# Performance work log

Hardware: AMD Instinct MI355X
Metric: run time of the kernel (lower is better)

Reference implementation:

```python
import jax, jax.numpy as jnp
from jax import lax
import numpy as np
import math

EPS = 1e-5
NBINS = 17   # quantized color levels round(x*255/16) for x in [0,1)
K_MODE = 11

def _bn(x, g, b):
    # BatchNorm2d in training mode: batch statistics over (B,H,W)
    m = jnp.mean(x, axis=(0, 2, 3), keepdims=True)
    v = jnp.var(x, axis=(0, 2, 3), keepdims=True)
    return (x - m) * lax.rsqrt(v + EPS) * g[None, :, None, None] + b[None, :, None, None]

def _lrelu(x):
    return jnp.where(x >= 0, x, 0.01 * x)

def _shared_conv(x, w, b, stride, padding):
    # one KxK kernel shared depthwise across all channels, scalar bias
    C = x.shape[1]
    k = jnp.tile(w[None, None], (C, 1, 1, 1))  # (C,1,K,K)
    y = lax.conv_general_dilated(x, k, (stride, stride),
                                 [(padding, padding), (padding, padding)],
                                 dimension_numbers=('NCHW', 'OIHW', 'NCHW'),
                                 feature_group_count=C)
    return y + b[0]

def _avg_pool_same(x, k):
    # avg_pool2d(k, stride=1, padding=k//2, count_include_pad=True)
    p = k // 2
    s = lax.reduce_window(x, 0.0, lax.add, (1, 1, k, k), (1, 1, 1, 1),
                          [(0, 0), (0, 0), (p, p), (p, p)])
    return s / float(k * k)

def _mode_pool(xq):
    # xq values are exact multiples of 16/256 -> recover integer bin index,
    # then mode over 11x11 window = argmax of per-bin counts (histogram).
    # torch zero-padding corresponds to bin 0; argmax first-max tie-break ->
    # smallest value, matching torch.mode.
    q = jnp.clip(jnp.round(xq * (256.0 / 16.0)).astype(jnp.int32), 0, NBINS - 1)
    pad = K_MODE // 2
    qp = jnp.pad(q, ((0, 0), (0, 0), (pad, pad), (pad, pad)))
    onehot = (qp[:, :, None] == jnp.arange(NBINS, dtype=jnp.int32)[None, None, :, None, None]).astype(jnp.float32)
    counts = lax.reduce_window(onehot, 0.0, lax.add, (1, 1, 1, K_MODE, K_MODE), (1, 1, 1, 1, 1), 'VALID')
    mode_bin = jnp.argmax(counts, axis=2)  # (B,C,H,W)
    return mode_bin.astype(xq.dtype) * (16.0 / 256.0)

def _forward(x, p_w1, p_b1, p_dw1, p_db1, p_g1, p_be1,
             p_w2, p_b2, p_dw2, p_db2, p_g2, p_be2,
             d_w, d_b, ia_w, ia_b, ia_g, ia_be,
             ib_w, ib_b, ib_g, ib_be,
             f_g1, f_be1, f_g2, f_be2):
    xq = jnp.round(x * (255.0 / 16.0)) * (16.0 / 256.0)
    xm = _mode_pool(xq)
    B, C, H, W = xm.shape
    half = p_w1.shape[0]

    # prepare: 1x1 conv -> depthwise 1x1 (per-channel scale) -> BN -> LeakyReLU, twice
    h = jnp.einsum('bchw,oc->bohw', xm, p_w1) + p_b1[None, :, None, None]
    h = h * p_dw1[None, :, None, None] + p_db1[None, :, None, None]
    h = _lrelu(_bn(h, p_g1, p_be1))
    h = jnp.einsum('bchw,oc->bohw', h, p_w2) + p_b2[None, :, None, None]
    h = h * p_dw2[None, :, None, None] + p_db2[None, :, None, None]
    h = _lrelu(_bn(h, p_g2, p_be2))

    n = int(math.floor(math.log(min(H, W), 3)))
    score = jnp.zeros((B, 2 * half, H, W), x.dtype)
    d = h
    for _ in range(n):
        d = _shared_conv(d, d_w, d_b, 3, 1)  # stride-3 downgrade
        z = jax.image.resize(d, (B, half, H, W), method='bilinear')
        a = _lrelu(_bn(_shared_conv(z, ia_w, ia_b, 1, 2), ia_g, ia_be))
        bb = _lrelu(_bn(_shared_conv(z, ib_w, ib_b, 1, 2), ib_g, ib_be))
        score = score + jnp.concatenate([a, bb], axis=1)  # Splitter + Stack(1)

    def ft(s):
        s = _bn(s, f_g1, f_be1)
        s = jnp.where(s > 0.1, 0.1 + 0.7 * (s - 0.1), s)  # MaxLeakyReLU(0.7, 0.1)
        s = _bn(s, f_g2, f_be2)
        return 2.0 * s - _avg_pool_same(s, K_MODE)  # EmphaseLocal(11): x + (x - local mean)

    score = ft(ft(ft(score)))
    return score / n

def setup_inputs() -> dict:
    key = jax.random.key(0)
    ks = jax.random.split(key, 32)
    B, Cin, H, W, half = 8, 3, 384, 384, 32
    r = lambda i, shp, s=0.1: s * jax.random.normal(ks[i], shp, dtype=jnp.float32)
    g = lambda i, shp: 1.0 + 0.1 * jax.random.normal(ks[i], shp, dtype=jnp.float32)
    return dict(
        x=jax.random.uniform(ks[0], (B, Cin, H, W), dtype=jnp.float32),
        p_w1=r(1, (half, Cin), 0.3), p_b1=r(2, (half,)),
        p_dw1=g(3, (half,)), p_db1=r(4, (half,)),
        p_g1=g(5, (half,)), p_be1=r(6, (half,)),
        p_w2=r(7, (half, half), 0.2), p_b2=r(8, (half,)),
        p_dw2=g(9, (half,)), p_db2=r(10, (half,)),
        p_g2=g(11, (half,)), p_be2=r(12, (half,)),
        d_w=r(13, (3, 3), 0.2), d_b=r(14, (1,)),
        ia_w=r(15, (5, 5), 0.2), ia_b=r(16, (1,)),
        ia_g=g(17, (half,)), ia_be=r(18, (half,)),
        ib_w=r(19, (5, 5), 0.2), ib_b=r(20, (1,)),
        ib_g=g(21, (half,)), ib_be=r(22, (half,)),
        f_g1=g(23, (2 * half,)), f_be1=r(24, (2 * half,)),
        f_g2=g(25, (2 * half,)), f_be2=r(26, (2 * half,)),
    )

def reference(x, p_w1, p_b1, p_dw1, p_db1, p_g1, p_be1,
              p_w2, p_b2, p_dw2, p_db2, p_g2, p_be2,
              d_w, d_b, ia_w, ia_b, ia_g, ia_be,
              ib_w, ib_b, ib_g, ib_be,
              f_g1, f_be1, f_g2, f_be2):
    return _forward(x, p_w1, p_b1, p_dw1, p_db1, p_g1, p_be1,
                    p_w2, p_b2, p_dw2, p_db2, p_g2, p_be2,
                    d_w, d_b, ia_w, ia_b, ia_g, ia_be,
                    ib_w, ib_b, ib_g, ib_be,
                    f_g1, f_be1, f_g2, f_be2)
```

## Files before the change

### kernel.cpp

```cpp
#include <hip/hip_runtime.h>

#define HW 147456
#define WID 384
#define NB 8
#define NPC 1179648
#define HW4 36864

static __device__ __forceinline__ float lrelu01(float v) { return v >= 0.f ? v : 0.01f * v; }
static __device__ __forceinline__ float mlrelu(float v) { return v > 0.1f ? 0.1f + 0.7f * (v - 0.1f) : v; }

__global__ __launch_bounds__(256) void mode_kernel(const float* __restrict__ x,
                                                   float* __restrict__ xm) {
  __shared__ unsigned char qt[26 * 76];
  __shared__ unsigned int cc[16 * 5 * 76];
  const int plane = blockIdx.z;
  const int x0 = blockIdx.x * 64;
  const int y0 = blockIdx.y * 16;
  const float* xp = x + (size_t)plane * HW;

  for (int i = threadIdx.x; i < 26 * 76; i += 256) {
    int r = i / 76, ccol = i - r * 76;
    int gy = y0 + r - 5, gx = x0 + ccol - 5;
    unsigned char q = 0;
    if (ccol < 74 && gy >= 0 && gy < WID && gx >= 0 && gx < WID) {
      float v = xp[gy * WID + gx];
      int qi = (int)rintf(v * 15.9375f);
      qi = qi < 0 ? 0 : (qi > 16 ? 16 : qi);
      q = (unsigned char)qi;
    }
    qt[i] = q;
  }
  __syncthreads();

  for (int i = threadIdx.x; i < 16 * 74; i += 256) {
    int yy = i / 74, col = i - yy * 74;
    unsigned int w0 = 0, w1 = 0, w2 = 0, w3 = 0, w4 = 0;
#pragma unroll
    for (int dy = 0; dy < 11; ++dy) {
      int q = qt[(yy + dy) * 76 + col];
      unsigned int inc = 1u << ((q & 3) << 3);
      int wsel = q >> 2;
      w0 += (wsel == 0) ? inc : 0u;
      w1 += (wsel == 1) ? inc : 0u;
      w2 += (wsel == 2) ? inc : 0u;
      w3 += (wsel == 3) ? inc : 0u;
      w4 += (wsel == 4) ? inc : 0u;
    }
    cc[(yy * 5 + 0) * 76 + col] = w0;
    cc[(yy * 5 + 1) * 76 + col] = w1;
    cc[(yy * 5 + 2) * 76 + col] = w2;
    cc[(yy * 5 + 3) * 76 + col] = w3;
    cc[(yy * 5 + 4) * 76 + col] = w4;
  }
  __syncthreads();

  for (int i = threadIdx.x; i < 16 * 64; i += 256) {
    int yy = i / 64, xx = i - yy * 64;
    unsigned int s0 = 0, s1 = 0, s2 = 0, s3 = 0, s4 = 0;
#pragma unroll
    for (int dx = 0; dx < 11; ++dx) {
      int col = xx + dx;
      s0 += cc[(yy * 5 + 0) * 76 + col];
      s1 += cc[(yy * 5 + 1) * 76 + col];
      s2 += cc[(yy * 5 + 2) * 76 + col];
      s3 += cc[(yy * 5 + 3) * 76 + col];
      s4 += cc[(yy * 5 + 4) * 76 + col];
    }
    unsigned int words[5] = {s0, s1, s2, s3, s4};
    int best = 0;
    unsigned int bc = s0 & 0xffu;
#pragma unroll
    for (int bin = 1; bin < 17; ++bin) {
      unsigned int cnt = (words[bin >> 2] >> ((bin & 3) * 8)) & 0xffu;
      if (cnt > bc) { bc = cnt; best = bin; }
    }
    xm[(size_t)plane * HW + (size_t)(y0 + yy) * WID + (x0 + xx)] = best * 0.0625f;
  }
}

__global__ __launch_bounds__(256) void xm_mom(const float4* __restrict__ X,
                                              float* __restrict__ part9) {
  float s0 = 0, s1 = 0, s2 = 0, m00 = 0, m01 = 0, m02 = 0, m11 = 0, m12 = 0, m22 = 0;
  const int end = (blockIdx.x + 1) * 1152;
  for (int u = blockIdx.x * 1152 + threadIdx.x; u < end; u += 256) {
    int b = u / HW4, p4 = u - b * HW4;
    const float4* base = X + (size_t)b * 3 * HW4 + p4;
    float4 a = base[0], bb = base[HW4], c = base[2 * HW4];
    s0 += a.x + a.y + a.z + a.w;
    s1 += bb.x + bb.y + bb.z + bb.w;
    s2 += c.x + c.y + c.z + c.w;
    m00 += a.x * a.x + a.y * a.y + a.z * a.z + a.w * a.w;
    m01 += a.x * bb.x + a.y * bb.y + a.z * bb.z + a.w * bb.w;
    m02 += a.x * c.x + a.y * c.y + a.z * c.z + a.w * c.w;
    m11 += bb.x * bb.x + bb.y * bb.y + bb.z * bb.z + bb.w * bb.w;
    m12 += bb.x * c.x + bb.y * c.y + bb.z * c.z + bb.w * c.w;
    m22 += c.x * c.x + c.y * c.y + c.z * c.z + c.w * c.w;
  }
  float vals[9] = {s0, s1, s2, m00, m01, m02, m11, m12, m22};
  int lane = threadIdx.x & 63, wd = threadIdx.x >> 6;
  __shared__ float red[4][9];
#pragma unroll
  for (int j = 0; j < 9; ++j) {
    float v = vals[j];
    for (int off = 32; off; off >>= 1) v += __shfl_down(v, off);
    if (lane == 0) red[wd][j] = v;
  }
  __syncthreads();
  if (threadIdx.x < 9)
    part9[blockIdx.x * 9 + threadIdx.x] =
        red[0][threadIdx.x] + red[1][threadIdx.x] + red[2][threadIdx.x] + red[3][threadIdx.x];
}

__global__ __launch_bounds__(64) void prep1_affine(const float* __restrict__ part9,
                                                   const float* __restrict__ w1,
                                                   const float* __restrict__ b1,
                                                   const float* __restrict__ dw1,
                                                   const float* __restrict__ db1,
                                                   const float* __restrict__ g,
                                                   const float* __restrict__ be,
                                                   float* __restrict__ sc,
                                                   float* __restrict__ sh) {
  __shared__ double M[9];
  if (threadIdx.x < 9) {
    double s = 0.0;
    for (int i = 0; i < 256; ++i) s += (double)part9[i * 9 + threadIdx.x];
    M[threadIdx.x] = s;
  }
  __syncthreads();
  if (threadIdx.x < 32) {
    int o = threadIdx.x;
    double dw = dw1[o];
    double a0 = (double)w1[o * 3] * dw, a1 = (double)w1[o * 3 + 1] * dw,
           a2 = (double)w1[o * 3 + 2] * dw;
    double k = (double)b1[o] * dw + (double)db1[o];
    double N = (double)NPC;
    double lin = (a0 * M[0] + a1 * M[1] + a2 * M[2]) / N;
    double mean = lin + k;
    double e2 = (a0 * a0 * M[3] + a1 * a1 * M[6] + a2 * a2 * M[8] +
                 2.0 * (a0 * a1 * M[4] + a0 * a2 * M[5] + a1 * a2 * M[7])) / N +
                2.0 * k * lin + k * k;
    double var = e2 - mean * mean;
    float rstd = rsqrtf((float)var + 1e-5f);
    float scl = rstd * g[o];
    sc[o] = scl;
    sh[o] = be[o] - (float)mean * scl;
  }
}

__global__ __launch_bounds__(256) void prep_fused(const float* __restrict__ xm,
                                                  const float* __restrict__ w1,
                                                  const float* __restrict__ b1,
                                                  const float* __restrict__ dw1,
                                                  const float* __restrict__ db1,
                                                  const float* __restrict__ P1SC,
                                                  const float* __restrict__ P1SH,
                                                  const float* __restrict__ w2,
                                                  const float* __restrict__ b2,
                                                  const float* __restrict__ dw2,
                                                  const float* __restrict__ db2,
                                                  float* __restrict__ t2,
                                                  float* __restrict__ part) {
  __shared__ float wl[1024];
  __shared__ float c1[32][4];
  __shared__ float bias2[32];
  __shared__ float wred[8][32];
  for (int i = threadIdx.x; i < 1024; i += 256) wl[i] = w2[i] * dw2[i >> 5];
  if (threadIdx.x < 32) {
    int o = threadIdx.x;
    float dw = dw1[o], s1 = P1SC[o];
    c1[o][0] = w1[o * 3] * dw * s1;
    c1[o][1] = w1[o * 3 + 1] * dw * s1;
    c1[o][2] = w1[o * 3 + 2] * dw * s1;
    c1[o][3] = (b1[o] * dw + db1[o]) * s1 + P1SH[o];
    bias2[o] = b2[o] * dw2[o] + db2[o];
  }
  __syncthreads();
  const int p0 = blockIdx.x * 512 + threadIdx.x;
  const int b = p0 / HW, pp = p0 - b * HW;
  const float* xb = xm + (size_t)b * 3 * HW + pp;
  float h[2][32];
#pragma unroll
  for (int q = 0; q < 2; ++q) {
    float x0 = xb[q * 256], x1 = xb[HW + q * 256], x2 = xb[2 * HW + q * 256];
#pragma unroll
    for (int o = 0; o < 32; ++o) {
      float u = fmaf(x0, c1[o][0], fmaf(x1, c1[o][1], fmaf(x2, c1[o][2], c1[o][3])));
      h[q][o] = lrelu01(u);
    }
  }
  float sv[32], sq[32];
  float* ob = t2 + (size_t)b * 32 * HW + pp;
  const float4* wl4 = reinterpret_cast<const float4*>(wl);
  for (int o = 0; o < 32; ++o) {
    float acc0 = bias2[o], acc1 = bias2[o];
#pragma unroll
    for (int c4 = 0; c4 < 8; ++c4) {
      float4 w4 = wl4[o * 8 + c4];
      int c = c4 * 4;
      acc0 = fmaf(h[0][c], w4.x, acc0);     acc1 = fmaf(h[1][c], w4.x, acc1);
      acc0 = fmaf(h[0][c + 1], w4.y, acc0); acc1 = fmaf(h[1][c + 1], w4.y, acc1);
      acc0 = fmaf(h[0][c + 2], w4.z, acc0); acc1 = fmaf(h[1][c + 2], w4.z, acc1);
      acc0 = fmaf(h[0][c + 3], w4.w, acc0); acc1 = fmaf(h[1][c + 3], w4.w, acc1);
    }
    ob[(size_t)o * HW] = acc0;
    ob[(size_t)o * HW + 256] = acc1;
    sv[o] = acc0 + acc1;
    sq[o] = acc0 * acc0 + acc1 * acc1;
  }
  int lane = threadIdx.x & 63, wd = threadIdx.x >> 6;
#pragma unroll
  for (int o = 0; o < 32; ++o) {
    float a = sv[o], q = sq[o];
    for (int off = 32; off; off >>= 1) {
      a += __shfl_down(a, off);
      q += __shfl_down(q, off);
    }
    if (lane == 0) { wred[wd][o] = a; wred[wd + 4][o] = q; }
  }
  __syncthreads();
  if (threadIdx.x < 32) {
    int o = threadIdx.x;
    part[((size_t)o * 2304 + blockIdx.x) * 2] = wred[0][o] + wred[1][o] + wred[2][o] + wred[3][o];
    part[((size_t)o * 2304 + blockIdx.x) * 2 + 1] = wred[4][o] + wred[5][o] + wred[6][o] + wred[7][o];
  }
}

__global__ __launch_bounds__(64) void stats_combine(const float* __restrict__ part, int nsplit,
                                                    const float* __restrict__ g,
                                                    const float* __restrict__ be,
                                                    float* __restrict__ sc,
                                                    float* __restrict__ sh) {
  const int c = blockIdx.x;
  double s = 0.0, q = 0.0;
  for (int i = threadIdx.x; i < nsplit; i += 64) {
    s += part[((size_t)c * nsplit + i) * 2];
    q += part[((size_t)c * nsplit + i) * 2 + 1];
  }
  for (int off = 32; off; off >>= 1) {
    s += __shfl_down(s, off);
    q += __shfl_down(q, off);
  }
  if (threadIdx.x == 0) {
    double mean = s / (double)NPC;
    double var = q / (double)NPC - mean * mean;
    float rstd = rsqrtf((float)var + 1e-5f);
    float scl = rstd * g[c];
    sc[c] = scl;
    sh[c] = be[c] - (float)mean * scl;
  }
}

template <bool AFF>
__global__ __launch_bounds__(256) void dconv(const float* __restrict__ in,
                                             const float* __restrict__ sc,
                                             const float* __restrict__ sh,
                                             const float* __restrict__ w9,
                                             const float* __restrict__ db,
                                             int Sin, int Sout,
                                             float* __restrict__ out, int total) {
  int idx = blockIdx.x * 256 + threadIdx.x;
  if (idx >= total) return;
  int xx = idx % Sout;
  int t = idx / Sout;
  int yy = t % Sout;
  int pc = t / Sout;
  int c = pc & 31;
  const float* ip = in + (size_t)pc * Sin * Sin;
  float a = AFF ? sc[c] : 1.f;
  float h = AFF ? sh[c] : 0.f;
  float acc = 0.f;
#pragma unroll
  for (int ky = 0; ky < 3; ++ky) {
    int iy = 3 * yy - 1 + ky;
    if (iy < 0 || iy >= Sin) continue;
#pragma unroll
    for (int kx = 0; kx < 3; ++kx) {
      int ix = 3 * xx - 1 + kx;
      if (ix < 0 || ix >= Sin) continue;
      float v = ip[(size_t)iy * Sin + ix];
      if (AFF) { v = v * a + h; v = lrelu01(v); }
      acc = fmaf(v, w9[ky * 3 + kx], acc);
    }
  }
  out[idx] = acc + db[0];
}

__device__ __forceinline__ void stage_geo2(int Sin, float scale, int tx, int ty,
                                           int* gx0, int* gx1, float* gfx, float* gxv,
                                           int* gy0, int* gy1, float* gfy, float* gyv) {
  if (threadIdx.x < 72) {
    int t = threadIdx.x >= 36 ? threadIdx.x - 36 : threadIdx.x;
    bool isY = threadIdx.x >= 36;
    int gp = (isY ? ty : tx) + t - 2;
    float valid = (gp >= 0 && gp < WID) ? 1.f : 0.f;
    int gpc = gp < 0 ? 0 : (gp >= WID ? WID - 1 : gp);
    float s = (gpc + 0.5f) * scale - 0.5f;
    float f0 = floorf(s);
    float fr = s - f0;
    int ii = (int)f0;
    int i1 = ii + 1 < Sin - 1 ? ii + 1 : Sin - 1;
    int i0 = ii > 0 ? ii : 0;
    if (isY) { gy0[t] = i0; gy1[t] = i1; gfy[t] = fr; gyv[t] = valid; }
    else     { gx0[t] = i0; gx1[t] = i1; gfx[t] = fr; gxv[t] = valid; }
  }
}

__device__ __forceinline__ void stage_sep(float* zt, float* dH, const float* dp, int Sin,
                                          const int* gx0, const int* gx1,
                                          const float* gfx, const float* gxv,
                                          const int* gy0, const int* gy1,
                                          const float* gfy, const float* gyv,
                                          int rowlo, int nrows) {
  for (int i = threadIdx.x; i < nrows * 36; i += 256) {
    int r = i / 36, zx = i - r * 36;
    const float* drow = dp + (size_t)(rowlo + r) * Sin;
    float v0 = drow[gx0[zx]], v1 = drow[gx1[zx]];
    dH[r * 40 + zx] = (v0 + gfx[zx] * (v1 - v0)) * gxv[zx];
  }
  __syncthreads();
  for (int i = threadIdx.x; i < 36 * 9; i += 256) {
    int zy = i / 9, k = i - zy * 9;
    int r0 = gy0[zy] - rowlo, r1 = gy1[zy] - rowlo;
    float fy = gfy[zy], vv = gyv[zy];
    float4 a = *reinterpret_cast<const float4*>(&dH[r0 * 40 + k * 4]);
    float4 b = *reinterpret_cast<const float4*>(&dH[r1 * 40 + k * 4]);
    float4 o;
    o.x = (a.x + fy * (b.x - a.x)) * vv;
    o.y = (a.y + fy * (b.y - a.y)) * vv;
    o.z = (a.z + fy * (b.z - a.z)) * vv;
    o.w = (a.w + fy * (b.w - a.w)) * vv;
    *reinterpret_cast<float4*>(&zt[zy * 40 + k * 4]) = o;
  }
}

__device__ __forceinline__ void conv_ab(const float* zt, int row, int g,
                                        const float* wa, const float* wb,
                                        float ba0, float bb0, float* A, float* Bv) {
  float aa0 = ba0, aa1 = ba0, aa2 = ba0, aa3 = ba0;
  float eb0 = bb0, eb1 = bb0, eb2 = bb0, eb3 = bb0;
#pragma unroll
  for (int dy = 0; dy < 5; ++dy) {
    const float* zr = &zt[(row + dy) * 40 + g * 4];
    float4 zlo = *reinterpret_cast<const float4*>(zr);
    float4 zhi = *reinterpret_cast<const float4*>(zr + 4);
    float z[8] = {zlo.x, zlo.y, zlo.z, zlo.w, zhi.x, zhi.y, zhi.z, zhi.w};
#pragma unroll
    for (int dx = 0; dx < 5; ++dx) {
      float wva = wa[dy * 5 + dx], wvb = wb[dy * 5 + dx];
      aa0 = fmaf(z[dx], wva, aa0);
      aa1 = fmaf(z[dx + 1], wva, aa1);
      aa2 = fmaf(z[dx + 2], wva, aa2);
      aa3 = fmaf(z[dx + 3], wva, aa3);
      eb0 = fmaf(z[dx], wvb, eb0);
      eb1 = fmaf(z[dx + 1], wvb, eb1);
      eb2 = fmaf(z[dx + 2], wvb, eb2);
      eb3 = fmaf(z[dx + 3], wvb, eb3);
    }
  }
  A[0] = aa0; A[1] = aa1; A[2] = aa2; A[3] = aa3;
  Bv[0] = eb0; Bv[1] = eb1; Bv[2] = eb2; Bv[3] = eb3;
}

__global__ __launch_bounds__(256) void upstats_all(const float* __restrict__ d1,
                                                   const float* __restrict__ d2,
                                                   const float* __restrict__ d3,
                                                   const float* __restrict__ d4,
                                                   const float* __restrict__ d5,
                                                   const float* __restrict__ wA5,
                                                   const float* __restrict__ wB5,
                                                   const float* __restrict__ bA,
                                                   const float* __restrict__ bB,
                                                   float* __restrict__ partA,
                                                   float* __restrict__ partB) {
  __shared__ __align__(16) float zt[36 * 40];
  __shared__ __align__(16) float dH[16 * 40];
  __shared__ int gx0[36], gx1[36], gy0[36], gy1[36];
  __shared__ float gfx[36], gfy[36], gxv[36], gyv[36];
  __shared__ float red[16];
  const int lvl = blockIdx.z;
  const float* dsel = lvl == 0 ? d1 : lvl == 1 ? d2 : lvl == 2 ? d3 : lvl == 3 ? d4 : d5;
  const int Sin = lvl == 0 ? 128 : lvl == 1 ? 43 : lvl == 2 ? 15 : lvl == 3 ? 5 : 2;
  const float scale = (float)Sin / 384.f;
  const int plane = blockIdx.y, tile = blockIdx.x;
  const int tx = (tile % 12) * 32, ty = (tile / 12) * 32;
  const float* dp = dsel + (size_t)plane * Sin * Sin;

  stage_geo2(Sin, scale, tx, ty, gx0, gx1, gfx, gxv, gy0, gy1, gfy, gyv);
  float wa[25], wb[25];
#pragma unroll
  for (int k = 0; k < 25; ++k) { wa[k] = wA5[k]; wb[k] = wB5[k]; }
  float ba0 = bA[0], bb0 = bB[0];
  __syncthreads();
  const int rowlo = gy0[0], nrows = gy1[35] - rowlo + 1;
  stage_sep(zt, dH, dp, Sin, gx0, gx1, gfx, gxv, gy0, gy1, gfy, gyv, rowlo, nrows);
  __syncthreads();

  float A[4], Bv[4];
  conv_ab(zt, threadIdx.x >> 3, threadIdx.x & 7, wa, wb, ba0, bb0, A, Bv);
  float sa = A[0] + A[1] + A[2] + A[3];
  float qa = A[0] * A[0] + A[1] * A[1] + A[2] * A[2] + A[3] * A[3];
  float sb = Bv[0] + Bv[1] + Bv[2] + Bv[3];
  float qb = Bv[0] * Bv[0] + Bv[1] * Bv[1] + Bv[2] * Bv[2] + Bv[3] * Bv[3];
  int lane = threadIdx.x & 63, wd = threadIdx.x >> 6;
  for (int off = 32; off; off >>= 1) {
    sa += __shfl_down(sa, off); qa += __shfl_down(qa, off);
    sb += __shfl_down(sb, off); qb += __shfl_down(qb, off);
  }
  if (lane == 0) {
    red[wd * 4] = sa; red[wd * 4 + 1] = qa;
    red[wd * 4 + 2] = sb; red[wd * 4 + 3] = qb;
  }
  __syncthreads();
  if (threadIdx.x == 0) {
    int b = plane >> 5, c = plane & 31;
    size_t pi = (size_t)lvl * 73728 + ((size_t)c * 1152 + (size_t)b * 144 + tile) * 2;
    partA[pi] = red[0] + red[4] + red[8] + red[12];
    partA[pi + 1] = red[1] + red[5] + red[9] + red[13];
    partB[pi] = red[2] + red[6] + red[10] + red[14];
    partB[pi + 1] = red[3] + red[7] + red[11] + red[15];
  }
}

__global__ __launch_bounds__(64) void combine_lvls(const float* __restrict__ partA,
                                                   const float* __restrict__ partB,
                                                   const float* __restrict__ ia_g,
                                                   const float* __restrict__ ia_be,
                                                   const float* __restrict__ ib_g,
                                                   const float* __restrict__ ib_be,
                                                   float* __restrict__ aff) {
  const int c = blockIdx.x, lvl = blockIdx.y, z = blockIdx.z;
  const float* part = (z ? partB : partA) + (size_t)lvl * 73728;
  const float* g = z ? ib_g : ia_g;
  const float* be = z ? ib_be : ia_be;
  double s = 0.0, q = 0.0;
  for (int i = threadIdx.x; i < 1152; i += 64) {
    s += part[((size_t)c * 1152 + i) * 2];
    q += part[((size_t)c * 1152 + i) * 2 + 1];
  }
  for (int off = 32; off; off >>= 1) {
    s += __shfl_down(s, off);
    q += __shfl_down(q, off);
  }
  if (threadIdx.x == 0) {
    double mean = s / (double)NPC;
    double var = q / (double)NPC - mean * mean;
    float rstd = rsqrtf((float)var + 1e-5f);
    float scl = rstd * g[c];
    aff[((z * 5 + lvl) * 2 + 0) * 32 + c] = scl;
    aff[((z * 5 + lvl) * 2 + 1) * 32 + c] = be[c] - (float)mean * scl;
  }
}

__global__ __launch_bounds__(256) void apply_all(const float* __restrict__ d1,
                                                 const float* __restrict__ d2,
                                                 const float* __restrict__ d3,
                                                 const float* __restrict__ d4,
                                                 const float* __restrict__ d5,
                                                 const float* __restrict__ wA5,
                                                 const float* __restrict__ wB5,
                                                 const float* __restrict__ bA,
                                                 const float* __restrict__ bB,
                                                 const float* __restrict__ aff,
                                                 float* __restrict__ outp,
                                                 float* __restrict__ partF) {
  __shared__ __align__(16) float zt[36 * 40];
  __shared__ __align__(16) float dH[16 * 40];
  __shared__ int gx0[36], gx1[36], gy0[36], gy1[36];
  __shared__ float gfx[36], gfy[36], gxv[36], gyv[36];
  __shared__ float red[16];
  const int plane = blockIdx.y, tile = blockIdx.x;
  const int tx = (tile % 12) * 32, ty = (tile / 12) * 32;
  const int b = plane >> 5, c = plane & 31;
  float wa[25], wb[25];
#pragma unroll
  for (int k = 0; k < 25; ++k) { wa[k] = wA5[k]; wb[k] = wB5[k]; }
  const float ba0 = bA[0], bb0 = bB[0];
  const int row = threadIdx.x >> 3, g = threadIdx.x & 7;

  float acA[4] = {0.f, 0.f, 0.f, 0.f}, acB[4] = {0.f, 0.f, 0.f, 0.f};
  for (int lvl = 0; lvl < 5; ++lvl) {
    const float* dsel = lvl == 0 ? d1 : lvl == 1 ? d2 : lvl == 2 ? d3 : lvl == 3 ? d4 : d5;
    const int Sin = lvl == 0 ? 128 : lvl == 1 ? 43 : lvl == 2 ? 15 : lvl == 3 ? 5 : 2;
    const float scale = (float)Sin / 384.f;
    const float* dp = dsel + (size_t)plane * Sin * Sin;
    __syncthreads();
    stage_geo2(Sin, scale, tx, ty, gx0, gx1, gfx, gxv, gy0, gy1, gfy, gyv);
    __syncthreads();
    const int rowlo = gy0[0], nrows = gy1[35] - rowlo + 1;
    stage_sep(zt, dH, dp, Sin, gx0, gx1, gfx, gxv, gy0, gy1, gfy, gyv, rowlo, nrows);
    __syncthreads();
    float A[4], Bv[4];
    conv_ab(zt, row, g, wa, wb, ba0, bb0, A, Bv);
    float as = aff[(lvl * 2 + 0) * 32 + c], ah = aff[(lvl * 2 + 1) * 32 + c];
    float bs = aff[((5 + lvl) * 2 + 0) * 32 + c], bh = aff[((5 + lvl) * 2 + 1) * 32 + c];
#pragma unroll
    for (int j = 0; j < 4; ++j) {
      acA[j] += lrelu01(fmaf(A[j], as, ah));
      acB[j] += lrelu01(fmaf(Bv[j], bs, bh));
    }
  }
  float4 xa = {acA[0], acA[1], acA[2], acA[3]};
  float4 xb = {acB[0], acB[1], acB[2], acB[3]};
  size_t po = (size_t)(b * 64 + c) * HW + (size_t)(ty + row) * WID + tx + g * 4;
  *reinterpret_cast<float4*>(outp + po) = xa;
  *reinterpret_cast<float4*>(outp + po + (size_t)32 * HW) = xb;

  float sa = xa.x + xa.y + xa.z + xa.w;
  float qa = xa.x * xa.x + xa.y * xa.y + xa.z * xa.z + xa.w * xa.w;
  float sb = xb.x + xb.y + xb.z + xb.w;
  float qb = xb.x * xb.x + xb.y * xb.y + xb.z * xb.z + xb.w * xb.w;
  int lane = threadIdx.x & 63, wd = threadIdx.x >> 6;
  for (int off = 32; off; off >>= 1) {
    sa += __shfl_down(sa, off); qa += __shfl_down(qa, off);
    sb += __shfl_down(sb, off); qb += __shfl_down(qb, off);
  }
  if (lane == 0) {
    red[wd * 4] = sa; red[wd * 4 + 1] = qa;
    red[wd * 4 + 2] = sb; red[wd * 4 + 3] = qb;
  }
  __syncthreads();
  if (threadIdx.x == 0) {
    size_t piA = ((size_t)c * 1152 + (size_t)b * 144 + tile) * 2;
    size_t piB = ((size_t)(c + 32) * 1152 + (size_t)b * 144 + tile) * 2;
    partF[piA] = red[0] + red[4] + red[8] + red[12];
    partF[piA + 1] = red[1] + red[5] + red[9] + red[13];
    partF[piB] = red[2] + red[6] + red[10] + red[14];
    partF[piB + 1] = red[3] + red[7] + red[11] + red[15];
  }
}

__global__ __launch_bounds__(256) void stats_mlrelu(const float4* __restrict__ X,
                                                    const float* __restrict__ sc1,
                                                    const float* __restrict__ sh1,
                                                    float* __restrict__ part) {
  int c = blockIdx.x >> 6, s = blockIdx.x & 63;
  float a1 = sc1[c], b1 = sh1[c];
  float sum = 0.f, sq = 0.f;
  int fi = s * 4608 + threadIdx.x;
#pragma unroll 2
  for (int it = 0; it < 18; ++it, fi += 256) {
    int b = fi / HW4, p4 = fi - b * HW4;
    float4 v = X[(size_t)(b * 64 + c) * HW4 + p4];
    float u;
    u = mlrelu(fmaf(v.x, a1, b1)); sum += u; sq += u * u;
    u = mlrelu(fmaf(v.y, a1, b1)); sum += u; sq += u * u;
    u = mlrelu(fmaf(v.z, a1, b1)); sum += u; sq += u * u;
    u = mlrelu(fmaf(v.w, a1, b1)); sum += u; sq += u * u;
  }
  int lane = threadIdx.x & 63, wd = threadIdx.x >> 6;
  for (int off = 32; off; off >>= 1) {
    sum += __shfl_down(sum, off);
    sq += __shfl_down(sq, off);
  }
  __shared__ float red[8];
  if (lane == 0) { red[wd * 2] = sum; red[wd * 2 + 1] = sq; }
  __syncthreads();
  if (threadIdx.x == 0) {
    part[((size_t)c * 64 + s) * 2] = red[0] + red[2] + red[4] + red[6];
    part[((size_t)c * 64 + s) * 2 + 1] = red[1] + red[3] + red[5] + red[7];
  }
}

__global__ __launch_bounds__(256) void ft_fused(const float* __restrict__ src,
                                                const float* __restrict__ F1SC,
                                                const float* __restrict__ F1SH,
                                                const float* __restrict__ F2SC,
                                                const float* __restrict__ F2SH,
                                                float* __restrict__ dst, float fscale,
                                                float* __restrict__ part) {
  __shared__ float sl[74 * 81];
  __shared__ __align__(16) float Hl[74 * 64];
  __shared__ float red[8];
  const int tile = blockIdx.x;
  const int plane = blockIdx.y;
  const int b = plane >> 6, c = plane & 63;
  const int tx = (tile % 6) * 64, ty = (tile / 6) * 64;
  const float a1 = F1SC[c], b1 = F1SH[c], a2 = F2SC[c], b2 = F2SH[c];
  const float* sp = src + (size_t)plane * HW;

  for (int i = threadIdx.x; i < 74 * 20; i += 256) {
    int r = i / 20, k = i - r * 20;
    int gy = ty + r - 5, gx = tx + k * 4 - 8;
    float4 sv = {0.f, 0.f, 0.f, 0.f};
    if (gy >= 0 && gy < WID && gx >= 0 && gx < WID) {
      float4 v = *reinterpret_cast<const float4*>(sp + (size_t)gy * WID + gx);
      sv.x = fmaf(mlrelu(fmaf(v.x, a1, b1)), a2, b2);
      sv.y = fmaf(mlrelu(fmaf(v.y, a1, b1)), a2, b2);
      sv.z = fmaf(mlrelu(fmaf(v.z, a1, b1)), a2, b2);
      sv.w = fmaf(mlrelu(fmaf(v.w, a1, b1)), a2, b2);
    }
    int base = r * 81 + k * 4;
    sl[base] = sv.x; sl[base + 1] = sv.y; sl[base + 2] = sv.z; sl[base + 3] = sv.w;
  }
  __syncthreads();

  for (int i = threadIdx.x; i < 74 * 16; i += 256) {
    int r = i >> 4, g = i & 15;
    const float* s0 = &sl[r * 81 + g * 4 + 3];
    float v[14];
#pragma unroll
    for (int j = 0; j < 14; ++j) v[j] = s0[j];
    float h0 = v[0] + v[1] + v[2] + v[3] + v[4] + v[5] + v[6] + v[7] + v[8] + v[9] + v[10];
    float h1 = h0 - v[0] + v[11];
    float h2 = h1 - v[1] + v[12];
    float h3 = h2 - v[2] + v[13];
    float4 hh = {h0, h1, h2, h3};
    *reinterpret_cast<float4*>(&Hl[r * 64 + g * 4]) = hh;
  }
  __syncthreads();

  const int g = threadIdx.x & 15, ly = threadIdx.x >> 4;
  const int y0 = ly * 4;
  const float4* H4 = reinterpret_cast<const float4*>(Hl);
  float4 acc = H4[y0 * 16 + g];
#pragma unroll
  for (int dy = 1; dy < 11; ++dy) {
    float4 t = H4[(y0 + dy) * 16 + g];
    acc.x += t.x; acc.y += t.y; acc.z += t.z; acc.w += t.w;
  }
  float sum = 0.f, sq = 0.f;
  float* dpo = dst + (size_t)plane * HW;
#pragma unroll
  for (int ry = 0; ry < 4; ++ry) {
    int y = y0 + ry;
    if (ry) {
      float4 ta = H4[(y + 10) * 16 + g];
      float4 tb = H4[(y - 1) * 16 + g];
      acc.x += ta.x - tb.x; acc.y += ta.y - tb.y;
      acc.z += ta.z - tb.z; acc.w += ta.w - tb.w;
    }
    const float* cp = &sl[(y + 5) * 81 + g * 4 + 8];
    float4 o;
    o.x = (2.f * cp[0] - acc.x * (1.f / 121.f)) * fscale;
    o.y = (2.f * cp[1] - acc.y * (1.f / 121.f)) * fscale;
    o.z = (2.f * cp[2] - acc.z * (1.f / 121.f)) * fscale;
    o.w = (2.f * cp[3] - acc.w * (1.f / 121.f)) * fscale;
    *reinterpret_cast<float4*>(dpo + (size_t)(ty + y) * WID + tx + g * 4) = o;
    sum += o.x + o.y + o.z + o.w;
    sq += o.x * o.x + o.y * o.y + o.z * o.z + o.w * o.w;
  }
  if (part) {
    int lane = threadIdx.x & 63, wd = threadIdx.x >> 6;
    for (int off = 32; off; off >>= 1) {
      sum += __shfl_down(sum, off);
      sq += __shfl_down(sq, off);
    }
    if (lane == 0) { red[wd * 2] = sum; red[wd * 2 + 1] = sq; }
    __syncthreads();
    if (threadIdx.x == 0) {
      size_t pi = ((size_t)c * 288 + (size_t)b * 36 + tile) * 2;
      part[pi] = red[0] + red[2] + red[4] + red[6];
      part[pi + 1] = red[1] + red[3] + red[5] + red[7];
    }
  }
}

extern "C" void kernel_launch(void* const* d_in, const int* in_sizes, int n_in,
                              void* d_out, int out_size, void* d_ws, size_t ws_size,
                              hipStream_t stream) {
  const float* x     = (const float*)d_in[0];
  const float* p_w1  = (const float*)d_in[1];
  const float* p_b1  = (const float*)d_in[2];
  const float* p_dw1 = (const float*)d_in[3];
  const float* p_db1 = (const float*)d_in[4];
  const float* p_g1  = (const float*)d_in[5];
  const float* p_be1 = (const float*)d_in[6];
  const float* p_w2  = (const float*)d_in[7];
  const float* p_b2  = (const float*)d_in[8];
  const float* p_dw2 = (const float*)d_in[9];
  const float* p_db2 = (const float*)d_in[10];
  const float* p_g2  = (const float*)d_in[11];
  const float* p_be2 = (const float*)d_in[12];
  const float* d_w   = (const float*)d_in[13];
  const float* d_b   = (const float*)d_in[14];
  const float* ia_w  = (const float*)d_in[15];
  const float* ia_b  = (const float*)d_in[16];
  const float* ia_g  = (const float*)d_in[17];
  const float* ia_be = (const float*)d_in[18];
  const float* ib_w  = (const float*)d_in[19];
  const float* ib_b  = (const float*)d_in[20];
  const float* ib_g  = (const float*)d_in[21];
  const float* ib_be = (const float*)d_in[22];
  const float* f_g1  = (const float*)d_in[23];
  const float* f_be1 = (const float*)d_in[24];
  const float* f_g2  = (const float*)d_in[25];
  const float* f_be2 = (const float*)d_in[26];
  float* out = (float*)d_out;
  float* ws = (float*)d_ws;

  const size_t SLOT = 37748736ull;
  float* B0 = ws;
  float* B1 = ws + 2 * SLOT;
  float* t2 = B0;
  float* partA = B0 + SLOT;
  float* partB = partA + 368640;
  float* partP = partB + 368640;
  float* part9 = partP + 147456;
  float* aff   = part9 + 2304;
  float* xm  = B1;
  float* dd1 = xm + 3538944;
  float* dd2 = dd1 + 4194304;
  float* dd3 = dd2 + 473344;
  float* dd4 = dd3 + 57600;
  float* dd5 = dd4 + 6400;
  float* partF = ws + 4 * SLOT;
  float* partS = partF + 147456;
  float* st    = partS + 8192;

  float* P1SC = st,       *P1SH = st + 32;
  float* P2SC = st + 64,  *P2SH = st + 96;
  float* F1SC = st + 128, *F1SH = st + 192;
  float* F2SC = st + 256, *F2SH = st + 320;

  mode_kernel<<<dim3(6, 24, 24), 256, 0, stream>>>(x, xm);
  xm_mom<<<256, 256, 0, stream>>>((const float4*)xm, part9);
  prep1_affine<<<1, 64, 0, stream>>>(part9, p_w1, p_b1, p_dw1, p_db1, p_g1, p_be1, P1SC, P1SH);
  prep_fused<<<2304, 256, 0, stream>>>(xm, p_w1, p_b1, p_dw1, p_db1, P1SC, P1SH,
                                       p_w2, p_b2, p_dw2, p_db2, t2, partP);
  stats_combine<<<32, 64, 0, stream>>>(partP, 2304, p_g2, p_be2, P2SC, P2SH);

  dconv<true><<<16384, 256, 0, stream>>>(t2, P2SC, P2SH, d_w, d_b, 384, 128, dd1,
                                         8 * 32 * 128 * 128);
  dconv<false><<<(8 * 32 * 43 * 43 + 255) / 256, 256, 0, stream>>>(
      dd1, nullptr, nullptr, d_w, d_b, 128, 43, dd2, 8 * 32 * 43 * 43);
  dconv<false><<<(8 * 32 * 15 * 15 + 255) / 256, 256, 0, stream>>>(
      dd2, nullptr, nullptr, d_w, d_b, 43, 15, dd3, 8 * 32 * 15 * 15);
  dconv<false><<<(8 * 32 * 5 * 5 + 255) / 256, 256, 0, stream>>>(
      dd3, nullptr, nullptr, d_w, d_b, 15, 5, dd4, 8 * 32 * 5 * 5);
  dconv<false><<<(8 * 32 * 2 * 2 + 255) / 256, 256, 0, stream>>>(
      dd4, nullptr, nullptr, d_w, d_b, 5, 2, dd5, 8 * 32 * 2 * 2);

  upstats_all<<<dim3(144, 256, 5), 256, 0, stream>>>(dd1, dd2, dd3, dd4, dd5,
                                                     ia_w, ib_w, ia_b, ib_b, partA, partB);
  combine_lvls<<<dim3(32, 5, 2), 64, 0, stream>>>(partA, partB, ia_g, ia_be, ib_g, ib_be, aff);
  apply_all<<<dim3(144, 256), 256, 0, stream>>>(dd1, dd2, dd3, dd4, dd5,
                                                ia_w, ib_w, ia_b, ib_b, aff, out, partF);

  const float* cur = out;
  float* dsts[3] = {B0, B1, out};
  for (int k = 0; k < 3; ++k) {
    stats_combine<<<64, 64, 0, stream>>>(partF, (k == 0) ? 1152 : 288, f_g1, f_be1, F1SC, F1SH);
    stats_mlrelu<<<64 * 64, 256, 0, stream>>>((const float4*)cur, F1SC, F1SH, partS);
    stats_combine<<<64, 64, 0, stream>>>(partS, 64, f_g2, f_be2, F2SC, F2SH);
    ft_fused<<<dim3(36, 512), 256, 0, stream>>>(cur, F1SC, F1SH, F2SC, F2SH, dsts[k],
                                                (k == 2) ? 0.2f : 1.0f,
                                                (k < 2) ? partF : nullptr);
    cur = dsts[k];
  }
}
```

Before: 2.131 ms.

## Merge pyramid stats and apply into one double-buffered, software-pipelined templated kernel

```diff
diff --git a/kernel.cpp b/kernel.cpp
--- a/kernel.cpp
+++ b/kernel.cpp
@@ -285,139 +285,234 @@
   out[idx] = acc + db[0];
 }
 
-__device__ __forceinline__ void stage_geo2(int Sin, float scale, int tx, int ty,
-                                           int* gx0, int* gx1, float* gfx, float* gxv,
-                                           int* gy0, int* gy1, float* gfy, float* gyv) {
-  if (threadIdx.x < 72) {
-    int t = threadIdx.x >= 36 ? threadIdx.x - 36 : threadIdx.x;
-    bool isY = threadIdx.x >= 36;
-    int gp = (isY ? ty : tx) + t - 2;
-    float valid = (gp >= 0 && gp < WID) ? 1.f : 0.f;
-    int gpc = gp < 0 ? 0 : (gp >= WID ? WID - 1 : gp);
-    float s = (gpc + 0.5f) * scale - 0.5f;
-    float f0 = floorf(s);
-    float fr = s - f0;
-    int ii = (int)f0;
-    int i1 = ii + 1 < Sin - 1 ? ii + 1 : Sin - 1;
-    int i0 = ii > 0 ? ii : 0;
-    if (isY) { gy0[t] = i0; gy1[t] = i1; gfy[t] = fr; gyv[t] = valid; }
-    else     { gx0[t] = i0; gx1[t] = i1; gfx[t] = fr; gxv[t] = valid; }
-  }
-}
-
-__device__ __forceinline__ void stage_sep(float* zt, float* dH, const float* dp, int Sin,
-                                          const int* gx0, const int* gx1,
-                                          const float* gfx, const float* gxv,
-                                          const int* gy0, const int* gy1,
-                                          const float* gfy, const float* gyv,
-                                          int rowlo, int nrows) {
-  for (int i = threadIdx.x; i < nrows * 36; i += 256) {
-    int r = i / 36, zx = i - r * 36;
-    const float* drow = dp + (size_t)(rowlo + r) * Sin;
-    float v0 = drow[gx0[zx]], v1 = drow[gx1[zx]];
-    dH[r * 40 + zx] = (v0 + gfx[zx] * (v1 - v0)) * gxv[zx];
-  }
-  __syncthreads();
-  for (int i = threadIdx.x; i < 36 * 9; i += 256) {
-    int zy = i / 9, k = i - zy * 9;
-    int r0 = gy0[zy] - rowlo, r1 = gy1[zy] - rowlo;
-    float fy = gfy[zy], vv = gyv[zy];
-    float4 a = *reinterpret_cast<const float4*>(&dH[r0 * 40 + k * 4]);
-    float4 b = *reinterpret_cast<const float4*>(&dH[r1 * 40 + k * 4]);
-    float4 o;
-    o.x = (a.x + fy * (b.x - a.x)) * vv;
-    o.y = (a.y + fy * (b.y - a.y)) * vv;
-    o.z = (a.z + fy * (b.z - a.z)) * vv;
-    o.w = (a.w + fy * (b.w - a.w)) * vv;
-    *reinterpret_cast<float4*>(&zt[zy * 40 + k * 4]) = o;
-  }
-}
-
-__device__ __forceinline__ void conv_ab(const float* zt, int row, int g,
-                                        const float* wa, const float* wb,
-                                        float ba0, float bb0, float* A, float* Bv) {
-  float aa0 = ba0, aa1 = ba0, aa2 = ba0, aa3 = ba0;
-  float eb0 = bb0, eb1 = bb0, eb2 = bb0, eb3 = bb0;
-#pragma unroll
-  for (int dy = 0; dy < 5; ++dy) {
-    const float* zr = &zt[(row + dy) * 40 + g * 4];
-    float4 zlo = *reinterpret_cast<const float4*>(zr);
-    float4 zhi = *reinterpret_cast<const float4*>(zr + 4);
-    float z[8] = {zlo.x, zlo.y, zlo.z, zlo.w, zhi.x, zhi.y, zhi.z, zhi.w};
-#pragma unroll
-    for (int dx = 0; dx < 5; ++dx) {
-      float wva = wa[dy * 5 + dx], wvb = wb[dy * 5 + dx];
-      aa0 = fmaf(z[dx], wva, aa0);
-      aa1 = fmaf(z[dx + 1], wva, aa1);
-      aa2 = fmaf(z[dx + 2], wva, aa2);
-      aa3 = fmaf(z[dx + 3], wva, aa3);
-      eb0 = fmaf(z[dx], wvb, eb0);
-      eb1 = fmaf(z[dx + 1], wvb, eb1);
-      eb2 = fmaf(z[dx + 2], wvb, eb2);
-      eb3 = fmaf(z[dx + 3], wvb, eb3);
-    }
-  }
-  A[0] = aa0; A[1] = aa1; A[2] = aa2; A[3] = aa3;
-  Bv[0] = eb0; Bv[1] = eb1; Bv[2] = eb2; Bv[3] = eb3;
-}
-
-__global__ __launch_bounds__(256) void upstats_all(const float* __restrict__ d1,
-                                                   const float* __restrict__ d2,
-                                                   const float* __restrict__ d3,
-                                                   const float* __restrict__ d4,
-                                                   const float* __restrict__ d5,
-                                                   const float* __restrict__ wA5,
-                                                   const float* __restrict__ wB5,
-                                                   const float* __restrict__ bA,
-                                                   const float* __restrict__ bB,
-                                                   float* __restrict__ partA,
-                                                   float* __restrict__ partB) {
-  __shared__ __align__(16) float zt[36 * 40];
-  __shared__ __align__(16) float dH[16 * 40];
-  __shared__ int gx0[36], gx1[36], gy0[36], gy1[36];
-  __shared__ float gfx[36], gfy[36], gxv[36], gyv[36];
-  __shared__ float red[16];
-  const int lvl = blockIdx.z;
-  const float* dsel = lvl == 0 ? d1 : lvl == 1 ? d2 : lvl == 2 ? d3 : lvl == 3 ? d4 : d5;
-  const int Sin = lvl == 0 ? 128 : lvl == 1 ? 43 : lvl == 2 ? 15 : lvl == 3 ? 5 : 2;
-  const float scale = (float)Sin / 384.f;
+static __device__ __forceinline__ int sin_of(int l) {
+  return l == 0 ? 128 : l == 1 ? 43 : l == 2 ? 15 : l == 3 ? 5 : 2;
+}
+
+template <bool APPLY>
+__global__ __launch_bounds__(256) void pyramid_k(
+    const float* __restrict__ d1, const float* __restrict__ d2,
+    const float* __restrict__ d3, const float* __restrict__ d4,
+    const float* __restrict__ d5,
+    const float* __restrict__ wA5, const float* __restrict__ wB5,
+    const float* __restrict__ bA, const float* __restrict__ bB,
+    const float* __restrict__ aff, float* __restrict__ outp,
+    float* __restrict__ partA, float* __restrict__ partB,
+    float* __restrict__ partF) {
+  __shared__ __align__(16) float zt[2][36 * 40];
+  __shared__ __align__(16) float dH[2][16 * 40];
+  __shared__ int gx0[2][36], gx1[2][36], gy0[2][36], gy1[2][36];
+  __shared__ float gfx[2][36], gfy[2][36], gxv[2][36], gyv[2][36];
+  __shared__ float red[80];
+  __shared__ int rowloS[2];
+
   const int plane = blockIdx.y, tile = blockIdx.x;
   const int tx = (tile % 12) * 32, ty = (tile / 12) * 32;
-  const float* dp = dsel + (size_t)plane * Sin * Sin;
-
-  stage_geo2(Sin, scale, tx, ty, gx0, gx1, gfx, gxv, gy0, gy1, gfy, gyv);
+  const int b = plane >> 5, c = plane & 31;
   float wa[25], wb[25];
 #pragma unroll
   for (int k = 0; k < 25; ++k) { wa[k] = wA5[k]; wb[k] = wB5[k]; }
-  float ba0 = bA[0], bb0 = bB[0];
-  __syncthreads();
-  const int rowlo = gy0[0], nrows = gy1[35] - rowlo + 1;
-  stage_sep(zt, dH, dp, Sin, gx0, gx1, gfx, gxv, gy0, gy1, gfy, gyv, rowlo, nrows);
-  __syncthreads();
-
-  float A[4], Bv[4];
-  conv_ab(zt, threadIdx.x >> 3, threadIdx.x & 7, wa, wb, ba0, bb0, A, Bv);
-  float sa = A[0] + A[1] + A[2] + A[3];
-  float qa = A[0] * A[0] + A[1] * A[1] + A[2] * A[2] + A[3] * A[3];
-  float sb = Bv[0] + Bv[1] + Bv[2] + Bv[3];
-  float qb = Bv[0] * Bv[0] + Bv[1] * Bv[1] + Bv[2] * Bv[2] + Bv[3] * Bv[3];
-  int lane = threadIdx.x & 63, wd = threadIdx.x >> 6;
-  for (int off = 32; off; off >>= 1) {
-    sa += __shfl_down(sa, off); qa += __shfl_down(qa, off);
-    sb += __shfl_down(sb, off); qb += __shfl_down(qb, off);
-  }
-  if (lane == 0) {
-    red[wd * 4] = sa; red[wd * 4 + 1] = qa;
-    red[wd * 4 + 2] = sb; red[wd * 4 + 3] = qb;
-  }
-  __syncthreads();
-  if (threadIdx.x == 0) {
-    int b = plane >> 5, c = plane & 31;
-    size_t pi = (size_t)lvl * 73728 + ((size_t)c * 1152 + (size_t)b * 144 + tile) * 2;
-    partA[pi] = red[0] + red[4] + red[8] + red[12];
-    partA[pi + 1] = red[1] + red[5] + red[9] + red[13];
-    partB[pi] = red[2] + red[6] + red[10] + red[14];
-    partB[pi + 1] = red[3] + red[7] + red[11] + red[15];
+  const float ba0 = bA[0], bb0 = bB[0];
+  const int row = threadIdx.x >> 3, g = threadIdx.x & 7;
+  const int lane = threadIdx.x & 63, wd = threadIdx.x >> 6;
+
+  float v0a, v1a, fxa, xva, v0b, v1b, fxb, xvb;
+  int offA, offB;
+  bool okA = false, okB = false;
+
+  auto plane_ptr = [&](int l) -> const float* {
+    const float* base = l == 0 ? d1 : l == 1 ? d2 : l == 2 ? d3 : l == 3 ? d4 : d5;
+    int Sin = sin_of(l);
+    return base + (size_t)plane * (Sin * Sin);
+  };
+
+  auto GEO = [&](int l, int s) {
+    int Sin = sin_of(l);
+    float scale = (float)Sin / 384.f;
+    if (threadIdx.x < 72) {
+      int t = threadIdx.x >= 36 ? threadIdx.x - 36 : threadIdx.x;
+      bool isY = threadIdx.x >= 36;
+      int gp = (isY ? ty : tx) + t - 2;
+      float valid = (gp >= 0 && gp < WID) ? 1.f : 0.f;
+      int gpc = gp < 0 ? 0 : (gp >= WID ? WID - 1 : gp);
+      float sp = (gpc + 0.5f) * scale - 0.5f;
+      float f0 = floorf(sp);
+      float fr = sp - f0;
+      int ii = (int)f0;
+      int i1 = ii + 1 < Sin - 1 ? ii + 1 : Sin - 1;
+      int i0 = ii > 0 ? ii : 0;
+      if (isY) {
+        gy0[s][t] = i0; gy1[s][t] = i1; gfy[s][t] = fr; gyv[s][t] = valid;
+        if (t == 0) rowloS[s] = i0;
+      } else {
+        gx0[s][t] = i0; gx1[s][t] = i1; gfx[s][t] = fr; gxv[s][t] = valid;
+      }
+    }
+  };
+
+  auto XISSUE = [&](int l, int s) {
+    int Sin = sin_of(l);
+    const float* dpl = plane_ptr(l);
+    int rl = rowloS[s];
+    int cnt = (gy1[s][35] - rl + 1) * 36;
+    int i = threadIdx.x;
+    okA = i < cnt;
+    if (okA) {
+      int r = i / 36, zx = i - r * 36;
+      const float* drow = dpl + (size_t)(rl + r) * Sin;
+      v0a = drow[gx0[s][zx]];
+      v1a = drow[gx1[s][zx]];
+      fxa = gfx[s][zx]; xva = gxv[s][zx];
+      offA = r * 40 + zx;
+    }
+    i += 256;
+    okB = i < cnt;
+    if (okB) {
+      int r = i / 36, zx = i - r * 36;
+      const float* drow = dpl + (size_t)(rl + r) * Sin;
+      v0b = drow[gx0[s][zx]];
+      v1b = drow[gx1[s][zx]];
+      fxb = gfx[s][zx]; xvb = gxv[s][zx];
+      offB = r * 40 + zx;
+    }
+  };
+
+  auto DHWRITE = [&](int s) {
+    if (okA) dH[s][offA] = (v0a + fxa * (v1a - v0a)) * xva;
+    if (okB) dH[s][offB] = (v0b + fxb * (v1b - v0b)) * xvb;
+  };
+
+  auto YINTERP = [&](int s) {
+    int rl = rowloS[s];
+    for (int i = threadIdx.x; i < 324; i += 256) {
+      int zy = i / 9, k = i - zy * 9;
+      int r0 = gy0[s][zy] - rl, r1 = gy1[s][zy] - rl;
+      float fy = gfy[s][zy], vv = gyv[s][zy];
+      float4 a4 = *reinterpret_cast<const float4*>(&dH[s][r0 * 40 + k * 4]);
+      float4 b4 = *reinterpret_cast<const float4*>(&dH[s][r1 * 40 + k * 4]);
+      float4 o;
+      o.x = (a4.x + fy * (b4.x - a4.x)) * vv;
+      o.y = (a4.y + fy * (b4.y - a4.y)) * vv;
+      o.z = (a4.z + fy * (b4.z - a4.z)) * vv;
+      o.w = (a4.w + fy * (b4.w - a4.w)) * vv;
+      *reinterpret_cast<float4*>(&zt[s][zy * 40 + k * 4]) = o;
+    }
+  };
+
+  GEO(0, 0);
+  __syncthreads();
+  XISSUE(0, 0);
+  DHWRITE(0);
+  GEO(1, 1);
+  __syncthreads();
+  YINTERP(0);
+  __syncthreads();
+
+  float acA[4] = {0.f, 0.f, 0.f, 0.f}, acB[4] = {0.f, 0.f, 0.f, 0.f};
+
+  for (int l = 0; l < 5; ++l) {
+    const int s = l & 1;
+    if (l < 4) XISSUE(l + 1, s ^ 1);
+
+    float A0 = ba0, A1 = ba0, A2 = ba0, A3 = ba0;
+    float B0 = bb0, B1 = bb0, B2 = bb0, B3 = bb0;
+#pragma unroll
+    for (int dy = 0; dy < 5; ++dy) {
+      const float* zr = &zt[s][(row + dy) * 40 + g * 4];
+      float4 zlo = *reinterpret_cast<const float4*>(zr);
+      float4 zhi = *reinterpret_cast<const float4*>(zr + 4);
+      float z[8] = {zlo.x, zlo.y, zlo.z, zlo.w, zhi.x, zhi.y, zhi.z, zhi.w};
+#pragma unroll
+      for (int dx = 0; dx < 5; ++dx) {
+        float wva = wa[dy * 5 + dx], wvb = wb[dy * 5 + dx];
+        A0 = fmaf(z[dx], wva, A0);
+        A1 = fmaf(z[dx + 1], wva, A1);
+        A2 = fmaf(z[dx + 2], wva, A2);
+        A3 = fmaf(z[dx + 3], wva, A3);
+        B0 = fmaf(z[dx], wvb, B0);
+        B1 = fmaf(z[dx + 1], wvb, B1);
+        B2 = fmaf(z[dx + 2], wvb, B2);
+        B3 = fmaf(z[dx + 3], wvb, B3);
+      }
+    }
+
+    if (APPLY) {
+      float as = aff[(l * 2 + 0) * 32 + c], ah = aff[(l * 2 + 1) * 32 + c];
+      float bs = aff[((5 + l) * 2 + 0) * 32 + c], bh = aff[((5 + l) * 2 + 1) * 32 + c];
+      acA[0] += lrelu01(fmaf(A0, as, ah));
+      acA[1] += lrelu01(fmaf(A1, as, ah));
+      acA[2] += lrelu01(fmaf(A2, as, ah));
+      acA[3] += lrelu01(fmaf(A3, as, ah));
+      acB[0] += lrelu01(fmaf(B0, bs, bh));
+      acB[1] += lrelu01(fmaf(B1, bs, bh));
+      acB[2] += lrelu01(fmaf(B2, bs, bh));
+      acB[3] += lrelu01(fmaf(B3, bs, bh));
+    } else {
+      float sa = A0 + A1 + A2 + A3;
+      float qa = A0 * A0 + A1 * A1 + A2 * A2 + A3 * A3;
+      float sb = B0 + B1 + B2 + B3;
+      float qb = B0 * B0 + B1 * B1 + B2 * B2 + B3 * B3;
+      for (int off = 32; off; off >>= 1) {
+        sa += __shfl_down(sa, off); qa += __shfl_down(qa, off);
+        sb += __shfl_down(sb, off); qb += __shfl_down(qb, off);
+      }
+      if (lane == 0) {
+        red[l * 16 + wd * 4 + 0] = sa;
+        red[l * 16 + wd * 4 + 1] = qa;
+        red[l * 16 + wd * 4 + 2] = sb;
+        red[l * 16 + wd * 4 + 3] = qb;
+      }
+    }
+
+    if (l < 4) DHWRITE(s ^ 1);
+    if (l < 3) GEO(l + 2, s);
+    if (l < 4) {
+      __syncthreads();
+      YINTERP(s ^ 1);
+      __syncthreads();
+    }
+  }
+
+  if (APPLY) {
+    float4 xa = {acA[0], acA[1], acA[2], acA[3]};
+    float4 xb = {acB[0], acB[1], acB[2], acB[3]};
+    size_t po = (size_t)(b * 64 + c) * HW + (size_t)(ty + row) * WID + tx + g * 4;
+    *reinterpret_cast<float4*>(outp + po) = xa;
+    *reinterpret_cast<float4*>(outp + po + (size_t)32 * HW) = xb;
+    float sa = xa.x + xa.y + xa.z + xa.w;
+    float qa = xa.x * xa.x + xa.y * xa.y + xa.z * xa.z + xa.w * xa.w;
+    float sb = xb.x + xb.y + xb.z + xb.w;
+    float qb = xb.x * xb.x + xb.y * xb.y + xb.z * xb.z + xb.w * xb.w;
+    for (int off = 32; off; off >>= 1) {
+      sa += __shfl_down(sa, off); qa += __shfl_down(qa, off);
+      sb += __shfl_down(sb, off); qb += __shfl_down(qb, off);
+    }
+    if (lane == 0) {
+      red[wd * 4 + 0] = sa; red[wd * 4 + 1] = qa;
+      red[wd * 4 + 2] = sb; red[wd * 4 + 3] = qb;
+    }
+    __syncthreads();
+    if (threadIdx.x == 0) {
+      size_t piA = ((size_t)c * 1152 + (size_t)b * 144 + tile) * 2;
+      size_t piB = ((size_t)(c + 32) * 1152 + (size_t)b * 144 + tile) * 2;
+      partF[piA] = red[0] + red[4] + red[8] + red[12];
+      partF[piA + 1] = red[1] + red[5] + red[9] + red[13];
+      partF[piB] = red[2] + red[6] + red[10] + red[14];
+      partF[piB + 1] = red[3] + red[7] + red[11] + red[15];
+    }
+  } else {
+    __syncthreads();
+    if (threadIdx.x < 5) {
+      int l = threadIdx.x;
+      const float* rl_ = &red[l * 16];
+      float SA = rl_[0] + rl_[4] + rl_[8] + rl_[12];
+      float QA = rl_[1] + rl_[5] + rl_[9] + rl_[13];
+      float SB = rl_[2] + rl_[6] + rl_[10] + rl_[14];
+      float QB = rl_[3] + rl_[7] + rl_[11] + rl_[15];
+      size_t pi = (size_t)l * 73728 + ((size_t)c * 1152 + (size_t)b * 144 + tile) * 2;
+      partA[pi] = SA; partA[pi + 1] = QA;
+      partB[pi] = SB; partB[pi + 1] = QB;
+    }
   }
 }
 
@@ -451,84 +546,6 @@
   }
 }
 
-__global__ __launch_bounds__(256) void apply_all(const float* __restrict__ d1,
-                                                 const float* __restrict__ d2,
-                                                 const float* __restrict__ d3,
-                                                 const float* __restrict__ d4,
-                                                 const float* __restrict__ d5,
-                                                 const float* __restrict__ wA5,
-                                                 const float* __restrict__ wB5,
-                                                 const float* __restrict__ bA,
-                                                 const float* __restrict__ bB,
-                                                 const float* __restrict__ aff,
-                                                 float* __restrict__ outp,
-                                                 float* __restrict__ partF) {
-  __shared__ __align__(16) float zt[36 * 40];
-  __shared__ __align__(16) float dH[16 * 40];
-  __shared__ int gx0[36], gx1[36], gy0[36], gy1[36];
-  __shared__ float gfx[36], gfy[36], gxv[36], gyv[36];
-  __shared__ float red[16];
-  const int plane = blockIdx.y, tile = blockIdx.x;
-  const int tx = (tile % 12) * 32, ty = (tile / 12) * 32;
-  const int b = plane >> 5, c = plane & 31;
-  float wa[25], wb[25];
-#pragma unroll
-  for (int k = 0; k < 25; ++k) { wa[k] = wA5[k]; wb[k] = wB5[k]; }
-  const float ba0 = bA[0], bb0 = bB[0];
-  const int row = threadIdx.x >> 3, g = threadIdx.x & 7;
-
-  float acA[4] = {0.f, 0.f, 0.f, 0.f}, acB[4] = {0.f, 0.f, 0.f, 0.f};
-  for (int lvl = 0; lvl < 5; ++lvl) {
-    const float* dsel = lvl == 0 ? d1 : lvl == 1 ? d2 : lvl == 2 ? d3 : lvl == 3 ? d4 : d5;
-    const int Sin = lvl == 0 ? 128 : lvl == 1 ? 43 : lvl == 2 ? 15 : lvl == 3 ? 5 : 2;
-    const float scale = (float)Sin / 384.f;
-    const float* dp = dsel + (size_t)plane * Sin * Sin;
-    __syncthreads();
-    stage_geo2(Sin, scale, tx, ty, gx0, gx1, gfx, gxv, gy0, gy1, gfy, gyv);
-    __syncthreads();
-    const int rowlo = gy0[0], nrows = gy1[35] - rowlo + 1;
-    stage_sep(zt, dH, dp, Sin, gx0, gx1, gfx, gxv, gy0, gy1, gfy, gyv, rowlo, nrows);
-    __syncthreads();
-    float A[4], Bv[4];
-    conv_ab(zt, row, g, wa, wb, ba0, bb0, A, Bv);
-    float as = aff[(lvl * 2 + 0) * 32 + c], ah = aff[(lvl * 2 + 1) * 32 + c];
-    float bs = aff[((5 + lvl) * 2 + 0) * 32 + c], bh = aff[((5 + lvl) * 2 + 1) * 32 + c];
-#pragma unroll
-    for (int j = 0; j < 4; ++j) {
-      acA[j] += lrelu01(fmaf(A[j], as, ah));
-      acB[j] += lrelu01(fmaf(Bv[j], bs, bh));
-    }
-  }
-  float4 xa = {acA[0], acA[1], acA[2], acA[3]};
-  float4 xb = {acB[0], acB[1], acB[2], acB[3]};
-  size_t po = (size_t)(b * 64 + c) * HW + (size_t)(ty + row) * WID + tx + g * 4;
-  *reinterpret_cast<float4*>(outp + po) = xa;
-  *reinterpret_cast<float4*>(outp + po + (size_t)32 * HW) = xb;
-
-  float sa = xa.x + xa.y + xa.z + xa.w;
-  float qa = xa.x * xa.x + xa.y * xa.y + xa.z * xa.z + xa.w * xa.w;
-  float sb = xb.x + xb.y + xb.z + xb.w;
-  float qb = xb.x * xb.x + xb.y * xb.y + xb.z * xb.z + xb.w * xb.w;
-  int lane = threadIdx.x & 63, wd = threadIdx.x >> 6;
-  for (int off = 32; off; off >>= 1) {
-    sa += __shfl_down(sa, off); qa += __shfl_down(qa, off);
-    sb += __shfl_down(sb, off); qb += __shfl_down(qb, off);
-  }
-  if (lane == 0) {
-    red[wd * 4] = sa; red[wd * 4 + 1] = qa;
-    red[wd * 4 + 2] = sb; red[wd * 4 + 3] = qb;
-  }
-  __syncthreads();
-  if (threadIdx.x == 0) {
-    size_t piA = ((size_t)c * 1152 + (size_t)b * 144 + tile) * 2;
-    size_t piB = ((size_t)(c + 32) * 1152 + (size_t)b * 144 + tile) * 2;
-    partF[piA] = red[0] + red[4] + red[8] + red[12];
-    partF[piA + 1] = red[1] + red[5] + red[9] + red[13];
-    partF[piB] = red[2] + red[6] + red[10] + red[14];
-    partF[piB + 1] = red[3] + red[7] + red[11] + red[15];
-  }
-}
-
 __global__ __launch_bounds__(256) void stats_mlrelu(const float4* __restrict__ X,
                                                     const float* __restrict__ sc1,
                                                     const float* __restrict__ sh1,
@@ -536,11 +553,11 @@
   int c = blockIdx.x >> 6, s = blockIdx.x & 63;
   float a1 = sc1[c], b1 = sh1[c];
   float sum = 0.f, sq = 0.f;
-  int fi = s * 4608 + threadIdx.x;
-#pragma unroll 2
-  for (int it = 0; it < 18; ++it, fi += 256) {
-    int b = fi / HW4, p4 = fi - b * HW4;
-    float4 v = X[(size_t)(b * 64 + c) * HW4 + p4];
+  int b = s >> 3;
+  const float4* Xp = X + (size_t)(b * 64 + c) * HW4 + (s & 7) * 4608 + threadIdx.x;
+#pragma unroll 6
+  for (int it = 0; it < 18; ++it) {
+    float4 v = Xp[it * 256];
     float u;
     u = mlrelu(fmaf(v.x, a1, b1)); sum += u; sq += u * u;
     u = mlrelu(fmaf(v.y, a1, b1)); sum += u; sq += u * u;
@@ -730,11 +747,13 @@
   dconv<false><<<(8 * 32 * 2 * 2 + 255) / 256, 256, 0, stream>>>(
       dd4, nullptr, nullptr, d_w, d_b, 5, 2, dd5, 8 * 32 * 2 * 2);
 
-  upstats_all<<<dim3(144, 256, 5), 256, 0, stream>>>(dd1, dd2, dd3, dd4, dd5,
-                                                     ia_w, ib_w, ia_b, ib_b, partA, partB);
+  pyramid_k<false><<<dim3(144, 256), 256, 0, stream>>>(
+      dd1, dd2, dd3, dd4, dd5, ia_w, ib_w, ia_b, ib_b,
+      nullptr, nullptr, partA, partB, nullptr);
   combine_lvls<<<dim3(32, 5, 2), 64, 0, stream>>>(partA, partB, ia_g, ia_be, ib_g, ib_be, aff);
-  apply_all<<<dim3(144, 256), 256, 0, stream>>>(dd1, dd2, dd3, dd4, dd5,
-                                                ia_w, ib_w, ia_b, ib_b, aff, out, partF);
+  pyramid_k<true><<<dim3(144, 256), 256, 0, stream>>>(
+      dd1, dd2, dd3, dd4, dd5, ia_w, ib_w, ia_b, ib_b,
+      aff, out, nullptr, nullptr, partF);
 
   const float* cur = out;
   float* dsts[3] = {B0, B1, out};
```

Result: slower. 2.416 ms (+13.4%).
